# Kernel tuning notes

Hardware: AMD Instinct MI355X
Metric: run time of the kernel (lower is better)

## Reference

```python
import jax, jax.numpy as jnp
import numpy as np

H = 16
D_MODEL = 1024
HEAD_DIM = D_MODEL // H
NEG = -1e9


def setup_inputs() -> dict:
    key = jax.random.key(0)
    k1, k2, k3, k4, k5, k6 = jax.random.split(key, 6)
    B, L = 2, 2048
    feature = jax.random.normal(k1, (B, L, D_MODEL), dtype=jnp.float32)
    mask = jax.random.randint(k2, (B, L), 0, 2, dtype=jnp.int32)
    # Linear weights stored torch-style as [out, in]; biases zero-init per initialize().
    s = 1.0 / np.sqrt(D_MODEL)
    W_Q = jax.random.uniform(k3, (D_MODEL, D_MODEL), jnp.float32, -s, s)
    W_K = jax.random.uniform(k4, (D_MODEL, D_MODEL), jnp.float32, -s, s)
    W_V = jax.random.uniform(k5, (D_MODEL, D_MODEL), jnp.float32, -s, s)
    b_Q = jnp.zeros((D_MODEL,), jnp.float32)
    b_K = jnp.zeros((D_MODEL,), jnp.float32)
    b_V = jnp.zeros((D_MODEL,), jnp.float32)
    return {"feature": feature, "mask": mask, "W_Q": W_Q, "b_Q": b_Q,
            "W_K": W_K, "b_K": b_K, "W_V": W_V, "b_V": b_V}


def reference(feature, mask, W_Q, b_Q, W_K, b_K, W_V, b_V):
    B, L, _ = feature.shape
    scale = jnp.sqrt(jnp.float32(HEAD_DIM))
    # Projections: torch Linear is x @ W^T + b. Split into heads: [B, H, L, Dh]
    def proj(W, b):
        y = feature @ W.T + b
        return y.reshape(B, L, H, HEAD_DIM).transpose(0, 2, 1, 3)
    Q = proj(W_Q, b_Q)
    K = proj(W_K, b_K)
    V = proj(W_V, b_V)
    # Scores [B, H, Lq, Lk]
    A = jnp.einsum('bhqd,bhkd->bhqk', Q, K) / scale
    # Key-side mask broadcast over heads and query positions
    A = jnp.where(mask[:, None, None, :] == 0, jnp.float32(NEG), A)
    alpha = jax.nn.softmax(A, axis=-1)
    out = jnp.einsum('bhqk,bhkd->bhqd', alpha, V)  # [B, H, L, Dh]
    return out.transpose(0, 2, 1, 3).reshape(B, L, H * HEAD_DIM)
```

## Files before the change

kernel.cpp:

```cpp
#include <hip/hip_runtime.h>

typedef __bf16 bf16;
typedef __attribute__((ext_vector_type(4))) __bf16 bf16x4;
typedef __attribute__((ext_vector_type(8))) __bf16 bf16x8;
typedef __attribute__((ext_vector_type(4))) float f32x4;
typedef __attribute__((ext_vector_type(16))) float f32x16;
typedef unsigned int u32;

#define D_MODEL 1024
#define SEQ_L   2048
#define NHEAD   16
#define HDIM    64
#define MROWS   4096

#define S_SCALE 0.18033688f

#define FEAT_OFF  512u
#define WQ_OFF    (FEAT_OFF + 4194304u)
#define WK_OFF    (WQ_OFF + 1048576u)
#define WV_OFF    (WK_OFF + 1048576u)
#define BQ_OFF    (WV_OFF + 1048576u)
#define BK_OFF    (BQ_OFF + 1024u)
#define BV_OFF    (BK_OFF + 1024u)
#define Q_OFF     (BV_OFF + 1024u)
#define K_OFF     (Q_OFF + 4194304u)
#define V_OFF     (K_OFF + 4194304u)

typedef const __attribute__((address_space(1))) u32* gp_t;
typedef __attribute__((address_space(3))) u32* lp_t;
__device__ __forceinline__ void ld16(const bf16* g, bf16* l) {
    __builtin_amdgcn_global_load_lds((gp_t)g, (lp_t)l, 16, 0, 0);
}

__global__ void convert_in(const float* __restrict__ feat,
                           const float* __restrict__ wq, const float* __restrict__ wk,
                           const float* __restrict__ wv,
                           const float* __restrict__ bq, const float* __restrict__ bk,
                           const float* __restrict__ bv,
                           bf16* __restrict__ ws) {
    const int bid = blockIdx.x;
    const float* src; bf16* dst; int off; float sc = 1.0f;
    if (bid < 4096)      { src = feat; dst = ws + FEAT_OFF; off = bid * 1024; }
    else if (bid < 5120) { src = wq;   dst = ws + WQ_OFF;   off = (bid - 4096) * 1024; sc = S_SCALE; }
    else if (bid < 6144) { src = wk;   dst = ws + WK_OFF;   off = (bid - 5120) * 1024; }
    else if (bid < 7168) { src = wv;   dst = ws + WV_OFF;   off = (bid - 6144) * 1024; }
    else if (bid == 7168){ src = bq;   dst = ws + BQ_OFF;   off = 0; sc = S_SCALE; }
    else if (bid == 7169){ src = bk;   dst = ws + BK_OFF;   off = 0; }
    else                 { src = bv;   dst = ws + BV_OFF;   off = 0; }
    int idx = off + threadIdx.x * 4;
    float4 v = *(const float4*)(src + idx);
    bf16x4 o;
    o[0] = (bf16)(v.x * sc);
    o[1] = (bf16)(v.y * sc);
    o[2] = (bf16)(v.z * sc);
    o[3] = (bf16)(v.w * sc);
    *(bf16x4*)(dst + idx) = o;
}

__global__ __launch_bounds__(256, 2) void qkv_gemm(const bf16* __restrict__ ws,
                                                   bf16* __restrict__ wsw,
                                                   const int* __restrict__ mask) {
    __shared__ bf16 smem[32768];
    const int zi   = blockIdx.z;
    const int t    = threadIdx.x;
    const int lane = t & 63;
    const int wave = t >> 6;
    const int quad = lane >> 4;
    const int l16  = lane & 15;
    const int wrow = (wave >> 1) * 64;
    const int wcol = (wave & 1) * 64;

    if (zi == 0) {
        bf16* Ab = smem;
        bf16* Bq = smem + 8192;
        bf16* Bk = smem + 16384;
        const bf16* X   = ws + FEAT_OFF;
        const bf16* Wq  = ws + WQ_OFF;
        const bf16* Wk  = ws + WK_OFF;
        const int m0 = blockIdx.x * 128;
        const int n0 = blockIdx.y * 128;

        const int r4  = lane >> 2;
        const int sgq = (lane & 3) ^ ((lane >> 3) & 3);

        f32x4 aq[4][4], ak[4][4];
        for (int mi = 0; mi < 4; ++mi)
            for (int ni = 0; ni < 4; ++ni) {
                aq[mi][ni] = (f32x4){0.f, 0.f, 0.f, 0.f};
                ak[mi][ni] = (f32x4){0.f, 0.f, 0.f, 0.f};
            }

#define STAGEQK(bb, k0)                                                        \
    do {                                                                       \
        _Pragma("unroll")                                                      \
        for (int i = 0; i < 2; ++i) {                                          \
            int ch  = wave * 2 + i;                                            \
            int row = ch * 16 + r4;                                            \
            ld16(X  + (size_t)(m0 + row) * D_MODEL + (k0) + sgq * 8,           \
                 Ab + (bb) * 4096 + ch * 512);                                 \
            ld16(Wq + (size_t)(n0 + row) * D_MODEL + (k0) + sgq * 8,           \
                 Bq + (bb) * 4096 + ch * 512);                                 \
            ld16(Wk + (size_t)(n0 + row) * D_MODEL + (k0) + sgq * 8,           \
                 Bk + (bb) * 4096 + ch * 512);                                 \
        }                                                                      \
    } while (0)

        STAGEQK(0, 0);
        __syncthreads();

        int cur = 0;
        for (int k0 = 0; k0 < D_MODEL; k0 += 32) {
            if (k0 + 32 < D_MODEL) STAGEQK(cur ^ 1, k0 + 32);

            bf16x8 af[4], bq8[4], bk8[4];
#pragma unroll
            for (int mi = 0; mi < 4; ++mi) {
                int row  = wrow + mi * 16 + l16;
                int phys = quad ^ ((row >> 1) & 3);
                af[mi] = *(const bf16x8*)(&Ab[cur * 4096 + row * 32 + phys * 8]);
            }
#pragma unroll
            for (int ni = 0; ni < 4; ++ni) {
                int row  = wcol + ni * 16 + l16;
                int phys = quad ^ ((row >> 1) & 3);
                bq8[ni] = *(const bf16x8*)(&Bq[cur * 4096 + row * 32 + phys * 8]);
                bk8[ni] = *(const bf16x8*)(&Bk[cur * 4096 + row * 32 + phys * 8]);
            }
#pragma unroll
            for (int mi = 0; mi < 4; ++mi)
#pragma unroll
                for (int ni = 0; ni < 4; ++ni)
                    aq[mi][ni] = __builtin_amdgcn_mfma_f32_16x16x32_bf16(
                        af[mi], bq8[ni], aq[mi][ni], 0, 0, 0);
#pragma unroll
            for (int mi = 0; mi < 4; ++mi)
#pragma unroll
                for (int ni = 0; ni < 4; ++ni)
                    ak[mi][ni] = __builtin_amdgcn_mfma_f32_16x16x32_bf16(
                        af[mi], bk8[ni], ak[mi][ni], 0, 0, 0);

            __syncthreads();
            cur ^= 1;
        }
#undef STAGEQK

        bf16* Yq = wsw + Q_OFF;
        bf16* Yk = wsw + K_OFF;
        const bf16* bq = ws + BQ_OFF;
        const bf16* bk = ws + BK_OFF;
#pragma unroll
        for (int ni = 0; ni < 4; ++ni) {
            int col = n0 + wcol + ni * 16 + l16;
            float bqf = (float)bq[col];
            float bkf = (float)bk[col];
#pragma unroll
            for (int mi = 0; mi < 4; ++mi) {
                int rowb = m0 + wrow + mi * 16 + quad * 4;
#pragma unroll
                for (int r = 0; r < 4; ++r) {
                    Yq[(size_t)(rowb + r) * D_MODEL + col] = (bf16)(aq[mi][ni][r] + bqf);
                    float v = ak[mi][ni][r] + bkf;
                    if (mask[rowb + r] == 0) v = 0.f;
                    Yk[(size_t)(rowb + r) * D_MODEL + col] = (bf16)v;
                }
            }
        }
    } else {
        bf16* Ab = smem;
        bf16* Bb = smem + 16384;
        const bf16* Amat = ws + WV_OFF;
        const bf16* Bmat = ws + FEAT_OFF;
        const bf16* bias = ws + BV_OFF;
        bf16* Y = wsw + V_OFF;
        const int m0 = blockIdx.y * 128;
        const int n0 = blockIdx.x * 128;

        const int r8 = lane >> 3;
        const int sl = lane & 7;
        const int sg = sl ^ r8;

        f32x4 acc[4][4];
        for (int mi = 0; mi < 4; ++mi)
            for (int ni = 0; ni < 4; ++ni)
                acc[mi][ni] = (f32x4){0.f, 0.f, 0.f, 0.f};

#define STAGEV(bb, k0)                                                         \
    do {                                                                       \
        _Pragma("unroll")                                                      \
        for (int i = 0; i < 4; ++i) {                                          \
            int ch  = wave * 4 + i;                                            \
            int row = ch * 8 + r8;                                             \
            ld16(Amat + (size_t)(m0 + row) * D_MODEL + (k0) + sg * 8,          \
                 Ab + (bb) * 8192 + ch * 512);                                 \
            ld16(Bmat + (size_t)(n0 + row) * D_MODEL + (k0) + sg * 8,          \
                 Bb + (bb) * 8192 + ch * 512);                                 \
        }                                                                      \
    } while (0)

        STAGEV(0, 0);
        __syncthreads();

        int cur = 0;
        for (int k0 = 0; k0 < D_MODEL; k0 += 64) {
            if (k0 + 64 < D_MODEL) STAGEV(cur ^ 1, k0 + 64);

#pragma unroll
            for (int kk = 0; kk < 2; ++kk) {
                const int sgb = quad + kk * 4;
                bf16x8 af[4], bfr[4];
#pragma unroll
                for (int mi = 0; mi < 4; ++mi) {
                    int row = wrow + mi * 16 + l16;
                    af[mi] = *(const bf16x8*)(
                        &Ab[cur * 8192 + row * 64 + ((sgb ^ (row & 7)) << 3)]);
                }
#pragma unroll
                for (int ni = 0; ni < 4; ++ni) {
                    int row = wcol + ni * 16 + l16;
                    bfr[ni] = *(const bf16x8*)(
                        &Bb[cur * 8192 + row * 64 + ((sgb ^ (row & 7)) << 3)]);
                }
#pragma unroll
                for (int mi = 0; mi < 4; ++mi)
#pragma unroll
                    for (int ni = 0; ni < 4; ++ni)
                        acc[mi][ni] = __builtin_amdgcn_mfma_f32_16x16x32_bf16(
                            af[mi], bfr[ni], acc[mi][ni], 0, 0, 0);
            }

            __syncthreads();
            cur ^= 1;
        }
#undef STAGEV

#pragma unroll
        for (int mi = 0; mi < 4; ++mi) {
#pragma unroll
            for (int r = 0; r < 4; ++r) {
                int rowv = m0 + wrow + mi * 16 + quad * 4 + r;
                float bvf = (float)bias[rowv];
#pragma unroll
                for (int ni = 0; ni < 4; ++ni) {
                    int col = n0 + wcol + ni * 16 + l16;
                    float v = acc[mi][ni][r] + bvf;
                    if (mask[col] == 0) v = 0.f;
                    size_t addr = (size_t)(col >> 11) * 2097152u +
                                  (size_t)rowv * 2048u + (col & 2047);
                    Y[addr] = (bf16)v;
                }
            }
        }
    }
}

__global__ __launch_bounds__(512, 4) void attn_kernel(
    const bf16* __restrict__ ws,
    const int* __restrict__ mask, float* __restrict__ out) {
    const int bh  = blockIdx.x;
    const int qt  = blockIdx.y;
    const int b   = bh >> 4, h = bh & 15;
    const int t    = threadIdx.x;
    const int lane = t & 63;
    const int wave = t >> 6;
    const int qh   = wave & 3;
    const int kh   = wave >> 2;
    const int half = lane >> 5;
    const int l31  = lane & 31;
    const int kt0  = kh * 1024;

    __shared__ bf16 smem[32768];
    bf16* Kb = smem;
    bf16* Vb = smem + 16384;

    const bf16* Qh  = ws + Q_OFF + (size_t)(b * SEQ_L) * D_MODEL + h * HDIM;
    const bf16* Kh  = ws + K_OFF + (size_t)(b * SEQ_L) * D_MODEL + h * HDIM;
    const bf16* Vth = ws + V_OFF + (size_t)b * 2097152u + (size_t)(h * HDIM) * SEQ_L;

    int mvv[16];
#pragma unroll
    for (int i = 0; i < 16; ++i)
        mvv[i] = mask[b * SEQ_L + kt0 + i * 64 + lane];

    const int srow = (lane >> 3);
    const int sg   = (lane & 7) ^ srow;

#define STAGE(bb, kt)                                                          \
    do {                                                                       \
        _Pragma("unroll")                                                      \
        for (int i = 0; i < 2; ++i) {                                          \
            int row = i * 32 + qh * 8 + srow;                                  \
            ld16(Kh + (size_t)((kt) + row) * D_MODEL + sg * 8,                 \
                 Kb + (kh * 2 + (bb)) * 4096 + i * 2048 + qh * 512);           \
            ld16(Vth + (size_t)row * SEQ_L + (kt) + sg * 8,                    \
                 Vb + (kh * 2 + (bb)) * 4096 + i * 2048 + qh * 512);           \
        }                                                                      \
    } while (0)

    STAGE(0, kt0);

    int nm = 0;
#pragma unroll
    for (int i = 0; i < 16; ++i)
        nm += (int)__popcll(__ballot(mvv[i] != 0));

    const int qrow0 = qt * 128 + qh * 32;
    bf16x8 qf[4];
#pragma unroll
    for (int ks = 0; ks < 4; ++ks)
        qf[ks] = *(const bf16x8*)(Qh + (size_t)(qrow0 + l31) * D_MODEL
                                  + ks * 16 + half * 8);

    bf16x8 ones;
#pragma unroll
    for (int j = 0; j < 8; ++j) ones[j] = (bf16)1.0f;

    f32x16 o[2], lacc;
#pragma unroll
    for (int i = 0; i < 16; ++i) { o[0][i] = 0.f; o[1][i] = 0.f; lacc[i] = 0.f; }

    __syncthreads();

    int cur = 0;
    for (int it = 0; it < 16; ++it) {
        const int kt = kt0 + it * 64;
        if (it < 15) STAGE(cur ^ 1, kt + 64);

        const bf16* Kcur = Kb + (kh * 2 + cur) * 4096;
        f32x16 st[2];
        __builtin_amdgcn_s_setprio(1);
#pragma unroll
        for (int ktile = 0; ktile < 2; ++ktile) {
#pragma unroll
            for (int i = 0; i < 16; ++i) st[ktile][i] = 0.f;
#pragma unroll
            for (int ks = 0; ks < 4; ++ks) {
                const int row  = ktile * 32 + l31;
                const int slot = (ks * 2 + half) ^ (l31 & 7);
                bf16x8 kf = *(const bf16x8*)(&Kcur[row * 64 + slot * 8]);
                st[ktile] = __builtin_amdgcn_mfma_f32_32x32x16_bf16(
                    kf, qf[ks], st[ktile], 0, 0, 0);
            }
        }
        __builtin_amdgcn_s_setprio(0);

        bf16x4 pk[2][4];
#pragma unroll
        for (int ktile = 0; ktile < 2; ++ktile) {
#pragma unroll
            for (int g = 0; g < 4; ++g) {
                bf16x4 pkv;
#pragma unroll
                for (int j = 0; j < 4; ++j)
                    pkv[j] = (bf16)__builtin_amdgcn_exp2f(st[ktile][g * 4 + j]);
                pk[ktile][g] = pkv;
            }
        }

        bf16x8 pf[4];
#pragma unroll
        for (int ks = 0; ks < 4; ++ks) {
            const int k1 = ks & 1, kt2 = ks >> 1;
            uint2 a  = __builtin_bit_cast(uint2, pk[kt2][2 * k1]);
            uint2 bb = __builtin_bit_cast(uint2, pk[kt2][2 * k1 + 1]);
            uint2 keep, send;
            keep.x = half ? bb.x : a.x;  keep.y = half ? bb.y : a.y;
            send.x = half ? a.x : bb.x;  send.y = half ? a.y : bb.y;
            uint2 recv;
            recv.x = (unsigned)__shfl_xor((int)send.x, 32);
            recv.y = (unsigned)__shfl_xor((int)send.y, 32);
            uint4 frag;
            frag.x = half ? recv.x : keep.x;
            frag.y = half ? recv.y : keep.y;
            frag.z = half ? keep.x : recv.x;
            frag.w = half ? keep.y : recv.y;
            pf[ks] = __builtin_bit_cast(bf16x8, frag);
        }

        const bf16* Vcur = Vb + (kh * 2 + cur) * 4096;
        __builtin_amdgcn_s_setprio(1);
#pragma unroll
        for (int ks = 0; ks < 4; ++ks)
            lacc = __builtin_amdgcn_mfma_f32_32x32x16_bf16(pf[ks], ones, lacc, 0, 0, 0);
#pragma unroll
        for (int dt = 0; dt < 2; ++dt) {
#pragma unroll
            for (int ks = 0; ks < 4; ++ks) {
                const int row  = dt * 32 + l31;
                const int slot = (ks * 2 + half) ^ (l31 & 7);
                bf16x8 vf = *(const bf16x8*)(&Vcur[row * 64 + slot * 8]);
                o[dt] = __builtin_amdgcn_mfma_f32_32x32x16_bf16(
                    pf[ks], vf, o[dt], 0, 0, 0);
            }
        }
        __builtin_amdgcn_s_setprio(0);

        __syncthreads();
        cur ^= 1;
    }
#undef STAGE

    const float corr = (float)(1024 - nm);
    float* ex = (float*)smem;
    const int slot = qh * 64 + lane;
    if (kh == 1) {
#pragma unroll
        for (int r = 0; r < 16; ++r) {
            ex[r * 256 + slot]        = o[0][r];
            ex[(16 + r) * 256 + slot] = o[1][r];
            ex[(32 + r) * 256 + slot] = lacc[r] - corr;
        }
    }
    __syncthreads();
    if (kh == 0) {
#pragma unroll
        for (int r = 0; r < 16; ++r) {
            const int q32 = (r & 3) + 8 * (r >> 2) + 4 * half;
            const int q = qrow0 + q32;
            const size_t base = ((size_t)(b * SEQ_L + q)) * D_MODEL + h * HDIM;
            const float l  = (lacc[r] - corr) + ex[(32 + r) * 256 + slot];
            const float rl = 1.0f / fmaxf(l, 1e-30f);
            out[base + l31]      = (o[0][r] + ex[r * 256 + slot]) * rl;
            out[base + 32 + l31] = (o[1][r] + ex[(16 + r) * 256 + slot]) * rl;
        }
    }
}

extern "C" void kernel_launch(void* const* d_in, const int* in_sizes, int n_in,
                              void* d_out, int out_size, void* d_ws, size_t ws_size,
                              hipStream_t stream) {
    const float* feat = (const float*)d_in[0];
    const int*   mask = (const int*)d_in[1];
    const float* Wq = (const float*)d_in[2];
    const float* bq = (const float*)d_in[3];
    const float* Wk = (const float*)d_in[4];
    const float* bk = (const float*)d_in[5];
    const float* Wv = (const float*)d_in[6];
    const float* bv = (const float*)d_in[7];

    bf16* ws = (bf16*)d_ws;

    convert_in<<<7171, 256, 0, stream>>>(feat, Wq, Wk, Wv, bq, bk, bv, ws);

    dim3 g1(32, 8, 2);
    qkv_gemm<<<g1, 256, 0, stream>>>(ws, ws, mask);

    dim3 g2(2 * NHEAD, SEQ_L / 128);
    attn_kernel<<<g2, 512, 0, stream>>>(ws, mask, (float*)d_out);
}
```

Measured before the change: 162.8 us.

## Load K fragments directly into registers and halve attention LDS footprint

K tiles are no longer staged through shared memory. Each wave loads its K MFMA fragments straight from global memory into double-buffered register arrays, and the loop is unrolled by two to alternate those buffers. Only V goes through LDS, and the row-sum exchange now uses a small separate array, which cuts shared memory per block roughly in half. The aim is to remove LDS traffic and bank pressure for K and to allow more resident blocks, at the cost of extra VGPRs and less coalesced, redundant global K loads across the four query waves.

```diff
diff --git a/kernel.cpp b/kernel.cpp
--- a/kernel.cpp
+++ b/kernel.cpp
@@ -268,9 +268,9 @@
     const int l31  = lane & 31;
     const int kt0  = kh * 1024;
 
-    __shared__ bf16 smem[32768];
-    bf16* Kb = smem;
-    bf16* Vb = smem + 16384;
+    __shared__ bf16 Vs[2][2][4096];
+    __shared__ float exl[256];
+    bf16* Vsp = &Vs[0][0][0];
 
     const bf16* Qh  = ws + Q_OFF + (size_t)(b * SEQ_L) * D_MODEL + h * HDIM;
     const bf16* Kh  = ws + K_OFF + (size_t)(b * SEQ_L) * D_MODEL + h * HDIM;
@@ -284,19 +284,31 @@
     const int srow = (lane >> 3);
     const int sg   = (lane & 7) ^ srow;
 
-#define STAGE(bb, kt)                                                          \
+#define STAGE_V(bb, kt)                                                        \
     do {                                                                       \
         _Pragma("unroll")                                                      \
         for (int i = 0; i < 2; ++i) {                                          \
             int row = i * 32 + qh * 8 + srow;                                  \
-            ld16(Kh + (size_t)((kt) + row) * D_MODEL + sg * 8,                 \
-                 Kb + (kh * 2 + (bb)) * 4096 + i * 2048 + qh * 512);           \
             ld16(Vth + (size_t)row * SEQ_L + (kt) + sg * 8,                    \
-                 Vb + (kh * 2 + (bb)) * 4096 + i * 2048 + qh * 512);           \
+                 Vsp + (kh * 2 + (bb)) * 4096 + i * 2048 + qh * 512);          \
         }                                                                      \
     } while (0)
 
-    STAGE(0, kt0);
+#define KLOAD(dst, kt)                                                         \
+    do {                                                                       \
+        _Pragma("unroll")                                                      \
+        for (int kk = 0; kk < 8; ++kk) {                                       \
+            const int ktile = kk >> 2, ks = kk & 3;                            \
+            dst[kk] = *(const bf16x8*)(Kh +                                    \
+                (size_t)((kt) + ktile * 32 + l31) * D_MODEL +                  \
+                ks * 16 + half * 8);                                           \
+        }                                                                      \
+    } while (0)
+
+    bf16x8 kA[8], kB[8];
+
+    STAGE_V(0, kt0);
+    KLOAD(kA, kt0);
 
     int nm = 0;
 #pragma unroll
@@ -320,94 +332,104 @@
 
     __syncthreads();
 
-    int cur = 0;
-    for (int it = 0; it < 16; ++it) {
-        const int kt = kt0 + it * 64;
-        if (it < 15) STAGE(cur ^ 1, kt + 64);
-
-        const bf16* Kcur = Kb + (kh * 2 + cur) * 4096;
-        f32x16 st[2];
-        __builtin_amdgcn_s_setprio(1);
-#pragma unroll
-        for (int ktile = 0; ktile < 2; ++ktile) {
-#pragma unroll
-            for (int i = 0; i < 16; ++i) st[ktile][i] = 0.f;
-#pragma unroll
-            for (int ks = 0; ks < 4; ++ks) {
-                const int row  = ktile * 32 + l31;
-                const int slot = (ks * 2 + half) ^ (l31 & 7);
-                bf16x8 kf = *(const bf16x8*)(&Kcur[row * 64 + slot * 8]);
-                st[ktile] = __builtin_amdgcn_mfma_f32_32x32x16_bf16(
-                    kf, qf[ks], st[ktile], 0, 0, 0);
-            }
-        }
-        __builtin_amdgcn_s_setprio(0);
-
-        bf16x4 pk[2][4];
-#pragma unroll
-        for (int ktile = 0; ktile < 2; ++ktile) {
-#pragma unroll
-            for (int g = 0; g < 4; ++g) {
-                bf16x4 pkv;
-#pragma unroll
-                for (int j = 0; j < 4; ++j)
-                    pkv[j] = (bf16)__builtin_amdgcn_exp2f(st[ktile][g * 4 + j]);
-                pk[ktile][g] = pkv;
-            }
-        }
-
-        bf16x8 pf[4];
-#pragma unroll
-        for (int ks = 0; ks < 4; ++ks) {
-            const int k1 = ks & 1, kt2 = ks >> 1;
-            uint2 a  = __builtin_bit_cast(uint2, pk[kt2][2 * k1]);
-            uint2 bb = __builtin_bit_cast(uint2, pk[kt2][2 * k1 + 1]);
-            uint2 keep, send;
-            keep.x = half ? bb.x : a.x;  keep.y = half ? bb.y : a.y;
-            send.x = half ? a.x : bb.x;  send.y = half ? a.y : bb.y;
-            uint2 recv;
-            recv.x = (unsigned)__shfl_xor((int)send.x, 32);
-            recv.y = (unsigned)__shfl_xor((int)send.y, 32);
-            uint4 frag;
-            frag.x = half ? recv.x : keep.x;
-            frag.y = half ? recv.y : keep.y;
-            frag.z = half ? keep.x : recv.x;
-            frag.w = half ? keep.y : recv.y;
-            pf[ks] = __builtin_bit_cast(bf16x8, frag);
-        }
-
-        const bf16* Vcur = Vb + (kh * 2 + cur) * 4096;
-        __builtin_amdgcn_s_setprio(1);
-#pragma unroll
-        for (int ks = 0; ks < 4; ++ks)
-            lacc = __builtin_amdgcn_mfma_f32_32x32x16_bf16(pf[ks], ones, lacc, 0, 0, 0);
-#pragma unroll
-        for (int dt = 0; dt < 2; ++dt) {
-#pragma unroll
-            for (int ks = 0; ks < 4; ++ks) {
-                const int row  = dt * 32 + l31;
-                const int slot = (ks * 2 + half) ^ (l31 & 7);
-                bf16x8 vf = *(const bf16x8*)(&Vcur[row * 64 + slot * 8]);
-                o[dt] = __builtin_amdgcn_mfma_f32_32x32x16_bf16(
-                    pf[ks], vf, o[dt], 0, 0, 0);
-            }
-        }
-        __builtin_amdgcn_s_setprio(0);
-
-        __syncthreads();
-        cur ^= 1;
+#define ATTN_ITER(IT, KC, KN, BUF, PREF)                                       \
+    do {                                                                       \
+        const int kt = kt0 + (IT) * 64;                                        \
+        if (PREF) {                                                            \
+            STAGE_V((BUF) ^ 1, kt + 64);                                       \
+            KLOAD(KN, kt + 64);                                                \
+        }                                                                      \
+         \
+        f32x16 st[2];                                                          \
+        __builtin_amdgcn_s_setprio(1);                                         \
+        _Pragma("unroll")                                                      \
+        for (int ktile = 0; ktile < 2; ++ktile) {                              \
+            _Pragma("unroll")                                                  \
+            for (int i = 0; i < 16; ++i) st[ktile][i] = 0.f;                   \
+            _Pragma("unroll")                                                  \
+            for (int ks = 0; ks < 4; ++ks)                                     \
+                st[ktile] = __builtin_amdgcn_mfma_f32_32x32x16_bf16(           \
+                    KC[ktile * 4 + ks], qf[ks], st[ktile], 0, 0, 0);           \
+        }                                                                      \
+        __builtin_amdgcn_s_setprio(0);                                         \
+             \
+        bf16x4 pk[2][4];                                                       \
+        _Pragma("unroll")                                                      \
+        for (int ktile = 0; ktile < 2; ++ktile) {                              \
+            _Pragma("unroll")                                                  \
+            for (int g = 0; g < 4; ++g) {                                      \
+                bf16x4 pkv;                                                    \
+                _Pragma("unroll")                                              \
+                for (int j = 0; j < 4; ++j)                                    \
+                    pkv[j] = (bf16)__builtin_amdgcn_exp2f(st[ktile][g*4+j]);   \
+                pk[ktile][g] = pkv;                                            \
+            }                                                                  \
+        }                                                                      \
+                            \
+        bf16x8 pf[4];                                                          \
+        _Pragma("unroll")                                                      \
+        for (int ks = 0; ks < 4; ++ks) {                                       \
+            const int k1 = ks & 1, kt2 = ks >> 1;                              \
+            uint2 a  = __builtin_bit_cast(uint2, pk[kt2][2 * k1]);             \
+            uint2 bb = __builtin_bit_cast(uint2, pk[kt2][2 * k1 + 1]);         \
+            uint2 keep, send;                                                  \
+            keep.x = half ? bb.x : a.x;  keep.y = half ? bb.y : a.y;           \
+            send.x = half ? a.x : bb.x;  send.y = half ? a.y : bb.y;           \
+            uint2 recv;                                                        \
+            recv.x = (unsigned)__shfl_xor((int)send.x, 32);                    \
+            recv.y = (unsigned)__shfl_xor((int)send.y, 32);                    \
+            uint4 frag;                                                        \
+            frag.x = half ? recv.x : keep.x;                                   \
+            frag.y = half ? recv.y : keep.y;                                   \
+            frag.z = half ? keep.x : recv.x;                                   \
+            frag.w = half ? keep.y : recv.y;                                   \
+            pf[ks] = __builtin_bit_cast(bf16x8, frag);                         \
+        }                                                                      \
+                                                   \
+        const bf16* Vcur = Vsp + (kh * 2 + (BUF)) * 4096;                      \
+        __builtin_amdgcn_s_setprio(1);                                         \
+        _Pragma("unroll")                                                      \
+        for (int ks = 0; ks < 4; ++ks)                                         \
+            lacc = __builtin_amdgcn_mfma_f32_32x32x16_bf16(                    \
+                pf[ks], ones, lacc, 0, 0, 0);                                  \
+        _Pragma("unroll")                                                      \
+        for (int dt = 0; dt < 2; ++dt) {                                       \
+            _Pragma("unroll")                                                  \
+            for (int ks = 0; ks < 4; ++ks) {                                   \
+                const int row  = dt * 32 + l31;                                \
+                const int slot = (ks * 2 + half) ^ (l31 & 7);                  \
+                bf16x8 vf = *(const bf16x8*)(&Vcur[row * 64 + slot * 8]);      \
+                o[dt] = __builtin_amdgcn_mfma_f32_32x32x16_bf16(               \
+                    pf[ks], vf, o[dt], 0, 0, 0);                               \
+            }                                                                  \
+        }                                                                      \
+        __builtin_amdgcn_s_setprio(0);                                         \
+        __syncthreads();           \
+    } while (0)
+
+    for (int ith = 0; ith < 8; ++ith) {
+        ATTN_ITER(2 * ith,     kA, kB, 0, 1);
+        ATTN_ITER(2 * ith + 1, kB, kA, 1, (ith < 7));
     }
-#undef STAGE
+#undef ATTN_ITER
+#undef KLOAD
+#undef STAGE_V
 
     const float corr = (float)(1024 - nm);
-    float* ex = (float*)smem;
+    float* ex = (float*)Vsp;
     const int slot = qh * 64 + lane;
+    if (l31 == 0) {
+#pragma unroll
+        for (int r = 0; r < 16; ++r) {
+            const int q32 = (r & 3) + 8 * (r >> 2) + 4 * half;
+            exl[kh * 128 + qh * 32 + q32] = lacc[r] - corr;
+        }
+    }
     if (kh == 1) {
 #pragma unroll
         for (int r = 0; r < 16; ++r) {
             ex[r * 256 + slot]        = o[0][r];
             ex[(16 + r) * 256 + slot] = o[1][r];
-            ex[(32 + r) * 256 + slot] = lacc[r] - corr;
         }
     }
     __syncthreads();
@@ -417,7 +439,7 @@
             const int q32 = (r & 3) + 8 * (r >> 2) + 4 * half;
             const int q = qrow0 + q32;
             const size_t base = ((size_t)(b * SEQ_L + q)) * D_MODEL + h * HDIM;
-            const float l  = (lacc[r] - corr) + ex[(32 + r) * 256 + slot];
+            const float l  = exl[qh * 32 + q32] + exl[128 + qh * 32 + q32];
             const float rl = 1.0f / fmaxf(l, 1e-30f);
             out[base + l31]      = (o[0][r] + ex[r * 256 + slot]) * rl;
             out[base + 32 + l31] = (o[1][r] + ex[(16 + r) * 256 + slot]) * rl;
```

New measurement: 313.9 us. +92.8%, slower.
